# Kernel tuning notes

Measured on AMD Instinct MI355X. Metric: run time of the kernel, lower is better.

The kernel has to match this reference:

```python
import jax, jax.numpy as jnp
import numpy as np

D = 256
NR_PATHS, PATH_LEN = 4096, 64
NR_NODES = 10000


def setup_inputs() -> dict:
    key = jax.random.key(0)
    ks = jax.random.split(key, 6)
    encoded_paths = jax.random.normal(ks[0], (NR_PATHS, PATH_LEN, D), dtype=jnp.float32)
    paths_mask = jax.random.randint(ks[1], (NR_PATHS, PATH_LEN), 0, 2).astype(jnp.bool_)
    paths_node_indices = jax.random.randint(ks[2], (NR_PATHS, PATH_LEN), 0, NR_NODES)
    previous_nodes_encodings = jax.random.normal(ks[3], (NR_NODES, D), dtype=jnp.float32)
    Wq = jax.random.normal(ks[4], (D, D), dtype=jnp.float32) / np.sqrt(D)
    gate_W = jax.random.normal(ks[5], (2 * D, D), dtype=jnp.float32) / np.sqrt(2 * D)
    gate_b = jnp.zeros((D,), dtype=jnp.float32)
    return {
        'encoded_paths': encoded_paths,
        'paths_mask': paths_mask,
        'paths_node_indices': paths_node_indices,
        'previous_nodes_encodings': previous_nodes_encodings,
        'Wq': Wq,
        'gate_W': gate_W,
        'gate_b': gate_b,
        'nr_nodes': NR_NODES,
    }


def _scatter_attn_combine(x, idx, m, queries, Wq, nr_nodes):
    # x: [N, D] flattened path-step encodings; idx: [N] target node; m: [N] bool mask
    d = x.shape[-1]
    q = queries @ Wq                                   # [nodes, D] attention queries
    scores = jnp.einsum('nd,nd->n', q[idx], x) / jnp.sqrt(jnp.asarray(d, x.dtype))
    scores = jnp.where(m, scores, jnp.asarray(-1e30, x.dtype))
    seg_max = jax.ops.segment_max(scores, idx, num_segments=nr_nodes)
    seg_max = jnp.where(jnp.isfinite(seg_max), seg_max, jnp.zeros_like(seg_max))
    e = jnp.exp(scores - seg_max[idx]) * m.astype(x.dtype)
    denom = jax.ops.segment_sum(e, idx, num_segments=nr_nodes)
    probs = e / jnp.maximum(denom[idx], jnp.asarray(1e-9, x.dtype))
    return jax.ops.segment_sum(probs[:, None] * x, idx, num_segments=nr_nodes)


def reference(encoded_paths, paths_mask, paths_node_indices,
              previous_nodes_encodings, Wq, gate_W, gate_b, nr_nodes):
    d = encoded_paths.shape[-1]
    x = encoded_paths.reshape(-1, d)
    idx = paths_node_indices.reshape(-1)
    m = paths_mask.reshape(-1)
    # attention-weighted scatter of masked path-step encodings onto nodes
    update = _scatter_attn_combine(x, idx, m, previous_nodes_encodings, Wq, nr_nodes)
    # gated state update: g = sigmoid([prev; update] W + b); new = g*prev + (1-g)*update
    g = jax.nn.sigmoid(jnp.concatenate([previous_nodes_encodings, update], axis=-1) @ gate_W + gate_b)
    return g * previous_nodes_encodings + (1.0 - g) * update
```

## Files before the change

### kernel.cpp

```cpp
#include <hip/hip_runtime.h>

#define D 256
#define NPATHS 4096
#define PLEN 64
#define NSTEPS (NPATHS * PLEN)
#define NNODES 10000

__device__ __forceinline__ void fma4(float4& acc, float s, const float4& w) {
    acc.x += s * w.x; acc.y += s * w.y; acc.z += s * w.z; acc.w += s * w.w;
}

#define QR 8
__global__ __launch_bounds__(64) void k_query(const float* __restrict__ prev,
                                              const float* __restrict__ Wq,
                                              float* __restrict__ q) {
    const int lane = threadIdx.x;
    const int row0 = blockIdx.x * QR;
    const float4* W4 = reinterpret_cast<const float4*>(Wq);
    float4 acc[QR];
#pragma unroll
    for (int r = 0; r < QR; ++r) acc[r] = make_float4(0.f, 0.f, 0.f, 0.f);

    for (int k4 = 0; k4 < 64; ++k4) {
        float4 w0 = W4[(k4 * 4 + 0) * 64 + lane];
        float4 w1 = W4[(k4 * 4 + 1) * 64 + lane];
        float4 w2 = W4[(k4 * 4 + 2) * 64 + lane];
        float4 w3 = W4[(k4 * 4 + 3) * 64 + lane];
#pragma unroll
        for (int r = 0; r < QR; ++r) {
            float4 a = *reinterpret_cast<const float4*>(&prev[(size_t)(row0 + r) * D + k4 * 4]);
            fma4(acc[r], a.x, w0);
            fma4(acc[r], a.y, w1);
            fma4(acc[r], a.z, w2);
            fma4(acc[r], a.w, w3);
        }
    }
    float4* Q4 = reinterpret_cast<float4*>(q);
#pragma unroll
    for (int r = 0; r < QR; ++r) Q4[(size_t)(row0 + r) * 64 + lane] = acc[r];
}

__global__ __launch_bounds__(256) void k_count(const int* __restrict__ mask,
                                               const int* __restrict__ nidx,
                                               int* __restrict__ counts) {
    const int step = blockIdx.x * 256 + threadIdx.x;
    if (step >= NSTEPS) return;
    if (!mask[step]) return;
    atomicAdd(&counts[nidx[step]], 1);
}

__global__ __launch_bounds__(256) void k_scan(const int* __restrict__ counts,
                                              int* __restrict__ offsets,
                                              int* __restrict__ cursor) {
    const int tid = threadIdx.x;
    const int lane = tid & 63;
    const int w = tid >> 6;
    const int CH = 40;
    const int base = tid * CH;
    int s = 0;
    for (int i = 0; i < CH; ++i) {
        int j = base + i;
        if (j < NNODES) s += counts[j];
    }
    int v = s;
    for (int d = 1; d < 64; d <<= 1) {
        int t = __shfl_up(v, d);
        if (lane >= d) v += t;
    }
    __shared__ int wsum[4];
    if (lane == 63) wsum[w] = v;
    __syncthreads();
    int woff = 0;
    for (int i = 0; i < w; ++i) woff += wsum[i];
    int run = woff + v - s;
    for (int i = 0; i < CH; ++i) {
        int j = base + i;
        if (j < NNODES) {
            offsets[j] = run;
            cursor[j] = run;
            run += counts[j];
        }
    }
    if (tid == 255) offsets[NNODES] = run;
}

__global__ __launch_bounds__(256) void k_perm(const int* __restrict__ mask,
                                              const int* __restrict__ nidx,
                                              int* __restrict__ cursor,
                                              int* __restrict__ perm) {
    const int step = blockIdx.x * 256 + threadIdx.x;
    if (step >= NSTEPS) return;
    if (!mask[step]) return;
    const int node = nidx[step];
    int p = atomicAdd(&cursor[node], 1);
    perm[p] = step;
}

__global__ __launch_bounds__(256) void k_combine(const float* __restrict__ x,
                                                 const float* __restrict__ q,
                                                 const int* __restrict__ offsets,
                                                 const int* __restrict__ perm,
                                                 float* __restrict__ update) {
    const int wave = threadIdx.x >> 6;
    const int lane = threadIdx.x & 63;
    const int node = blockIdx.x * 4 + wave;
    if (node >= NNODES) return;
    const int off = offsets[node];
    const int cnt = offsets[node + 1] - off;

    const float4* x4 = reinterpret_cast<const float4*>(x);
    float4 qa = reinterpret_cast<const float4*>(q)[(size_t)node * 64 + lane];

    float4 acc = make_float4(0.f, 0.f, 0.f, 0.f);
    float m = -3.0e38f;
    float l = 0.f;

    for (int base = 0; base < cnt; base += 64) {
        const int lim = min(64, cnt - base);
        int myperm = perm[off + base + lane];

        float4 xs0, xs1;
        {
            int s0 = __shfl(myperm, 0);
            xs0 = x4[(size_t)s0 * 64 + lane];
        }
        if (lim > 1) {
            int s1 = __shfl(myperm, 1);
            xs1 = x4[(size_t)s1 * 64 + lane];
        }
        for (int i = 0; i < lim; ++i) {
            float4 cur = (i & 1) ? xs1 : xs0;
            if (i + 2 < lim) {
                int sn = __shfl(myperm, i + 2);
                float4 xn = x4[(size_t)sn * 64 + lane];
                if (i & 1) xs1 = xn; else xs0 = xn;
            }
            float s = cur.x * qa.x + cur.y * qa.y + cur.z * qa.z + cur.w * qa.w;
            s += __shfl_xor(s, 32);
            s += __shfl_xor(s, 16);
            s += __shfl_xor(s, 8);
            s += __shfl_xor(s, 4);
            s += __shfl_xor(s, 2);
            s += __shfl_xor(s, 1);
            s *= 0.0625f;

            float mn = fmaxf(m, s);
            float scale = __expf(m - mn);
            float wgt = __expf(s - mn);
            l = l * scale + wgt;
            acc.x = acc.x * scale + wgt * cur.x;
            acc.y = acc.y * scale + wgt * cur.y;
            acc.z = acc.z * scale + wgt * cur.z;
            acc.w = acc.w * scale + wgt * cur.w;
            m = mn;
        }
    }

    const float inv = 1.f / fmaxf(l, 1e-9f);
    float4 o = make_float4(acc.x * inv, acc.y * inv, acc.z * inv, acc.w * inv);
    reinterpret_cast<float4*>(update)[(size_t)node * 64 + lane] = o;
}

#define GR 8
__global__ __launch_bounds__(64) void k_gate(const float* __restrict__ prev,
                                             const float* __restrict__ update,
                                             const float* __restrict__ gW,
                                             const float* __restrict__ gb,
                                             float* __restrict__ out) {
    const int lane = threadIdx.x;
    const int row0 = blockIdx.x * GR;
    const float4* W4 = reinterpret_cast<const float4*>(gW);
    float4 acc[GR];
#pragma unroll
    for (int r = 0; r < GR; ++r) acc[r] = make_float4(0.f, 0.f, 0.f, 0.f);

    for (int k4 = 0; k4 < 64; ++k4) {
        float4 w0 = W4[(k4 * 4 + 0) * 64 + lane];
        float4 w1 = W4[(k4 * 4 + 1) * 64 + lane];
        float4 w2 = W4[(k4 * 4 + 2) * 64 + lane];
        float4 w3 = W4[(k4 * 4 + 3) * 64 + lane];
#pragma unroll
        for (int r = 0; r < GR; ++r) {
            float4 a = *reinterpret_cast<const float4*>(&prev[(size_t)(row0 + r) * D + k4 * 4]);
            fma4(acc[r], a.x, w0);
            fma4(acc[r], a.y, w1);
            fma4(acc[r], a.z, w2);
            fma4(acc[r], a.w, w3);
        }
    }
    for (int k4 = 0; k4 < 64; ++k4) {
        float4 w0 = W4[(256 + k4 * 4 + 0) * 64 + lane];
        float4 w1 = W4[(256 + k4 * 4 + 1) * 64 + lane];
        float4 w2 = W4[(256 + k4 * 4 + 2) * 64 + lane];
        float4 w3 = W4[(256 + k4 * 4 + 3) * 64 + lane];
#pragma unroll
        for (int r = 0; r < GR; ++r) {
            float4 a = *reinterpret_cast<const float4*>(&update[(size_t)(row0 + r) * D + k4 * 4]);
            fma4(acc[r], a.x, w0);
            fma4(acc[r], a.y, w1);
            fma4(acc[r], a.z, w2);
            fma4(acc[r], a.w, w3);
        }
    }
    const float4* P4 = reinterpret_cast<const float4*>(prev);
    const float4* U4 = reinterpret_cast<const float4*>(update);
    const float4 b4 = reinterpret_cast<const float4*>(gb)[lane];
    float4* O4 = reinterpret_cast<float4*>(out);
#pragma unroll
    for (int r = 0; r < GR; ++r) {
        const size_t ri = (size_t)(row0 + r) * 64 + lane;
        float4 p = P4[ri];
        float4 u = U4[ri];
        float gx = 1.f / (1.f + __expf(-(acc[r].x + b4.x)));
        float gy = 1.f / (1.f + __expf(-(acc[r].y + b4.y)));
        float gz = 1.f / (1.f + __expf(-(acc[r].z + b4.z)));
        float gw = 1.f / (1.f + __expf(-(acc[r].w + b4.w)));
        float4 o;
        o.x = gx * p.x + (1.f - gx) * u.x;
        o.y = gy * p.y + (1.f - gy) * u.y;
        o.z = gz * p.z + (1.f - gz) * u.z;
        o.w = gw * p.w + (1.f - gw) * u.w;
        O4[ri] = o;
    }
}

extern "C" void kernel_launch(void* const* d_in, const int* in_sizes, int n_in,
                              void* d_out, int out_size, void* d_ws, size_t ws_size,
                              hipStream_t stream) {
    const float* enc   = (const float*)d_in[0];
    const int*   mask  = (const int*)d_in[1];
    const int*   nidx  = (const int*)d_in[2];
    const float* prev  = (const float*)d_in[3];
    const float* Wq    = (const float*)d_in[4];
    const float* gW    = (const float*)d_in[5];
    const float* gb    = (const float*)d_in[6];
    float* out = (float*)d_out;

    char* ws = (char*)d_ws;
    float* q       = (float*)(ws + 0);
    int*   counts  = (int*)  (ws + 10240000);
    int*   offsets = (int*)  (ws + 10280192);
    int*   cursor  = (int*)  (ws + 10320640);
    int*   perm    = (int*)  (ws + 10360832);
    float* update  = (float*)(ws + 11409408);

    hipMemsetAsync(counts, 0, NNODES * sizeof(int), stream);

    k_query<<<NNODES / QR, 64, 0, stream>>>(prev, Wq, q);
    k_count<<<NSTEPS / 256, 256, 0, stream>>>(mask, nidx, counts);
    k_scan<<<1, 256, 0, stream>>>(counts, offsets, cursor);
    k_perm<<<NSTEPS / 256, 256, 0, stream>>>(mask, nidx, cursor, perm);
    k_combine<<<(NNODES + 3) / 4, 256, 0, stream>>>(enc, q, offsets, perm, update);
    k_gate<<<NNODES / GR, 64, 0, stream>>>(prev, update, gW, gb, out);
}
```

Baseline: 539.2 us.

## Batch combine loop by four, prefetch weight rows, fold count zeroing into query

The combine kernel now gathers and processes four path-step rows per iteration, double-buffered, doing one online-softmax rescale per group of four instead of per row. This exposes more memory-level parallelism for the gathered loads and interleaves the shuffle reductions. The query and gate GEMV loops software-prefetch the next weight rows, and the counts memset is folded into the query kernel to drop one launch. The cost is higher register pressure from eight float4 buffers, plus masked padding loads at group tails.

```diff
diff --git a/kernel.cpp b/kernel.cpp
--- a/kernel.cpp
+++ b/kernel.cpp
@@ -13,19 +13,27 @@
 #define QR 8
 __global__ __launch_bounds__(64) void k_query(const float* __restrict__ prev,
                                               const float* __restrict__ Wq,
-                                              float* __restrict__ q) {
+                                              float* __restrict__ q,
+                                              int* __restrict__ counts) {
     const int lane = threadIdx.x;
     const int row0 = blockIdx.x * QR;
+    if (lane < QR) counts[blockIdx.x * QR + lane] = 0;
+
     const float4* W4 = reinterpret_cast<const float4*>(Wq);
     float4 acc[QR];
 #pragma unroll
     for (int r = 0; r < QR; ++r) acc[r] = make_float4(0.f, 0.f, 0.f, 0.f);
 
+    float4 w0 = W4[0 * 64 + lane];
+    float4 w1 = W4[1 * 64 + lane];
+    float4 w2 = W4[2 * 64 + lane];
+    float4 w3 = W4[3 * 64 + lane];
     for (int k4 = 0; k4 < 64; ++k4) {
-        float4 w0 = W4[(k4 * 4 + 0) * 64 + lane];
-        float4 w1 = W4[(k4 * 4 + 1) * 64 + lane];
-        float4 w2 = W4[(k4 * 4 + 2) * 64 + lane];
-        float4 w3 = W4[(k4 * 4 + 3) * 64 + lane];
+        const int nk = (k4 + 1) & 63;
+        float4 n0 = W4[(nk * 4 + 0) * 64 + lane];
+        float4 n1 = W4[(nk * 4 + 1) * 64 + lane];
+        float4 n2 = W4[(nk * 4 + 2) * 64 + lane];
+        float4 n3 = W4[(nk * 4 + 3) * 64 + lane];
 #pragma unroll
         for (int r = 0; r < QR; ++r) {
             float4 a = *reinterpret_cast<const float4*>(&prev[(size_t)(row0 + r) * D + k4 * 4]);
@@ -34,6 +42,7 @@
             fma4(acc[r], a.z, w2);
             fma4(acc[r], a.w, w3);
         }
+        w0 = n0; w1 = n1; w2 = n2; w3 = n3;
     }
     float4* Q4 = reinterpret_cast<float4*>(q);
 #pragma unroll
@@ -119,40 +128,59 @@
         const int lim = min(64, cnt - base);
         int myperm = perm[off + base + lane];
 
-        float4 xs0, xs1;
-        {
-            int s0 = __shfl(myperm, 0);
-            xs0 = x4[(size_t)s0 * 64 + lane];
-        }
-        if (lim > 1) {
-            int s1 = __shfl(myperm, 1);
-            xs1 = x4[(size_t)s1 * 64 + lane];
-        }
-        for (int i = 0; i < lim; ++i) {
-            float4 cur = (i & 1) ? xs1 : xs0;
-            if (i + 2 < lim) {
-                int sn = __shfl(myperm, i + 2);
-                float4 xn = x4[(size_t)sn * 64 + lane];
-                if (i & 1) xs1 = xn; else xs0 = xn;
+        auto ldg4 = [&](int i, float4& r0, float4& r1, float4& r2, float4& r3) {
+            int s0 = (i + 0 < lim) ? __shfl(myperm, i + 0) : 0;
+            int s1 = (i + 1 < lim) ? __shfl(myperm, i + 1) : 0;
+            int s2 = (i + 2 < lim) ? __shfl(myperm, i + 2) : 0;
+            int s3 = (i + 3 < lim) ? __shfl(myperm, i + 3) : 0;
+            r0 = x4[(size_t)s0 * 64 + lane];
+            r1 = x4[(size_t)s1 * 64 + lane];
+            r2 = x4[(size_t)s2 * 64 + lane];
+            r3 = x4[(size_t)s3 * 64 + lane];
+        };
+
+        auto proc4 = [&](int i, float4 r0, float4 r1, float4 r2, float4 r3) {
+            float s0 = r0.x * qa.x + r0.y * qa.y + r0.z * qa.z + r0.w * qa.w;
+            float s1 = r1.x * qa.x + r1.y * qa.y + r1.z * qa.z + r1.w * qa.w;
+            float s2 = r2.x * qa.x + r2.y * qa.y + r2.z * qa.z + r2.w * qa.w;
+            float s3 = r3.x * qa.x + r3.y * qa.y + r3.z * qa.z + r3.w * qa.w;
+#pragma unroll
+            for (int d = 32; d >= 1; d >>= 1) {
+                s0 += __shfl_xor(s0, d);
+                s1 += __shfl_xor(s1, d);
+                s2 += __shfl_xor(s2, d);
+                s3 += __shfl_xor(s3, d);
             }
-            float s = cur.x * qa.x + cur.y * qa.y + cur.z * qa.z + cur.w * qa.w;
-            s += __shfl_xor(s, 32);
-            s += __shfl_xor(s, 16);
-            s += __shfl_xor(s, 8);
-            s += __shfl_xor(s, 4);
-            s += __shfl_xor(s, 2);
-            s += __shfl_xor(s, 1);
-            s *= 0.0625f;
-
-            float mn = fmaxf(m, s);
-            float scale = __expf(m - mn);
-            float wgt = __expf(s - mn);
-            l = l * scale + wgt;
-            acc.x = acc.x * scale + wgt * cur.x;
-            acc.y = acc.y * scale + wgt * cur.y;
-            acc.z = acc.z * scale + wgt * cur.z;
-            acc.w = acc.w * scale + wgt * cur.w;
+            s0 = (i + 0 < lim) ? s0 * 0.0625f : -3.0e38f;
+            s1 = (i + 1 < lim) ? s1 * 0.0625f : -3.0e38f;
+            s2 = (i + 2 < lim) ? s2 * 0.0625f : -3.0e38f;
+            s3 = (i + 3 < lim) ? s3 * 0.0625f : -3.0e38f;
+            float mn = fmaxf(fmaxf(fmaxf(s0, s1), fmaxf(s2, s3)), m);
+            float sc = __expf(m - mn);
+            float e0 = __expf(s0 - mn);
+            float e1 = __expf(s1 - mn);
+            float e2 = __expf(s2 - mn);
+            float e3 = __expf(s3 - mn);
+            l = l * sc + ((e0 + e1) + (e2 + e3));
+            acc.x = acc.x * sc + ((e0 * r0.x + e1 * r1.x) + (e2 * r2.x + e3 * r3.x));
+            acc.y = acc.y * sc + ((e0 * r0.y + e1 * r1.y) + (e2 * r2.y + e3 * r3.y));
+            acc.z = acc.z * sc + ((e0 * r0.z + e1 * r1.z) + (e2 * r2.z + e3 * r3.z));
+            acc.w = acc.w * sc + ((e0 * r0.w + e1 * r1.w) + (e2 * r2.w + e3 * r3.w));
             m = mn;
+        };
+
+        float4 a0, a1, a2, a3, b0, b1, b2, b3;
+        int i = 0;
+        ldg4(0, a0, a1, a2, a3);
+        for (;;) {
+            if (i + 4 < lim) ldg4(i + 4, b0, b1, b2, b3);
+            proc4(i, a0, a1, a2, a3);
+            i += 4;
+            if (i >= lim) break;
+            if (i + 4 < lim) ldg4(i + 4, a0, a1, a2, a3);
+            proc4(i, b0, b1, b2, b3);
+            i += 4;
+            if (i >= lim) break;
         }
     }
 
@@ -174,32 +202,48 @@
 #pragma unroll
     for (int r = 0; r < GR; ++r) acc[r] = make_float4(0.f, 0.f, 0.f, 0.f);
 
-    for (int k4 = 0; k4 < 64; ++k4) {
-        float4 w0 = W4[(k4 * 4 + 0) * 64 + lane];
-        float4 w1 = W4[(k4 * 4 + 1) * 64 + lane];
-        float4 w2 = W4[(k4 * 4 + 2) * 64 + lane];
-        float4 w3 = W4[(k4 * 4 + 3) * 64 + lane];
-#pragma unroll
-        for (int r = 0; r < GR; ++r) {
-            float4 a = *reinterpret_cast<const float4*>(&prev[(size_t)(row0 + r) * D + k4 * 4]);
-            fma4(acc[r], a.x, w0);
-            fma4(acc[r], a.y, w1);
-            fma4(acc[r], a.z, w2);
-            fma4(acc[r], a.w, w3);
-        }
-    }
-    for (int k4 = 0; k4 < 64; ++k4) {
-        float4 w0 = W4[(256 + k4 * 4 + 0) * 64 + lane];
-        float4 w1 = W4[(256 + k4 * 4 + 1) * 64 + lane];
-        float4 w2 = W4[(256 + k4 * 4 + 2) * 64 + lane];
-        float4 w3 = W4[(256 + k4 * 4 + 3) * 64 + lane];
-#pragma unroll
-        for (int r = 0; r < GR; ++r) {
-            float4 a = *reinterpret_cast<const float4*>(&update[(size_t)(row0 + r) * D + k4 * 4]);
-            fma4(acc[r], a.x, w0);
-            fma4(acc[r], a.y, w1);
-            fma4(acc[r], a.z, w2);
-            fma4(acc[r], a.w, w3);
+    {
+        float4 w0 = W4[0 * 64 + lane];
+        float4 w1 = W4[1 * 64 + lane];
+        float4 w2 = W4[2 * 64 + lane];
+        float4 w3 = W4[3 * 64 + lane];
+        for (int k4 = 0; k4 < 64; ++k4) {
+            const int nk = (k4 + 1) & 63;
+            float4 n0 = W4[(nk * 4 + 0) * 64 + lane];
+            float4 n1 = W4[(nk * 4 + 1) * 64 + lane];
+            float4 n2 = W4[(nk * 4 + 2) * 64 + lane];
+            float4 n3 = W4[(nk * 4 + 3) * 64 + lane];
+#pragma unroll
+            for (int r = 0; r < GR; ++r) {
+                float4 a = *reinterpret_cast<const float4*>(&prev[(size_t)(row0 + r) * D + k4 * 4]);
+                fma4(acc[r], a.x, w0);
+                fma4(acc[r], a.y, w1);
+                fma4(acc[r], a.z, w2);
+                fma4(acc[r], a.w, w3);
+            }
+            w0 = n0; w1 = n1; w2 = n2; w3 = n3;
+        }
+    }
+    {
+        float4 w0 = W4[(256 + 0) * 64 + lane];
+        float4 w1 = W4[(256 + 1) * 64 + lane];
+        float4 w2 = W4[(256 + 2) * 64 + lane];
+        float4 w3 = W4[(256 + 3) * 64 + lane];
+        for (int k4 = 0; k4 < 64; ++k4) {
+            const int nk = (k4 + 1) & 63;
+            float4 n0 = W4[(256 + nk * 4 + 0) * 64 + lane];
+            float4 n1 = W4[(256 + nk * 4 + 1) * 64 + lane];
+            float4 n2 = W4[(256 + nk * 4 + 2) * 64 + lane];
+            float4 n3 = W4[(256 + nk * 4 + 3) * 64 + lane];
+#pragma unroll
+            for (int r = 0; r < GR; ++r) {
+                float4 a = *reinterpret_cast<const float4*>(&update[(size_t)(row0 + r) * D + k4 * 4]);
+                fma4(acc[r], a.x, w0);
+                fma4(acc[r], a.y, w1);
+                fma4(acc[r], a.z, w2);
+                fma4(acc[r], a.w, w3);
+            }
+            w0 = n0; w1 = n1; w2 = n2; w3 = n3;
         }
     }
     const float4* P4 = reinterpret_cast<const float4*>(prev);
@@ -244,9 +288,7 @@
     int*   perm    = (int*)  (ws + 10360832);
     float* update  = (float*)(ws + 11409408);
 
-    hipMemsetAsync(counts, 0, NNODES * sizeof(int), stream);
-
-    k_query<<<NNODES / QR, 64, 0, stream>>>(prev, Wq, q);
+    k_query<<<NNODES / QR, 64, 0, stream>>>(prev, Wq, q, counts);
     k_count<<<NSTEPS / 256, 256, 0, stream>>>(mask, nidx, counts);
     k_scan<<<1, 256, 0, stream>>>(counts, offsets, cursor);
     k_perm<<<NSTEPS / 256, 256, 0, stream>>>(mask, nidx, cursor, perm);
```

After: 529.4 us. No clear change (-1.8%).
